# Optimization experiments

Hardware: AMD Instinct MI355X
Metric: run time of the kernel (lower is better)

Reference implementation:

```python
import jax, jax.numpy as jnp
import numpy as np

N_HEADS = 16


def setup_inputs() -> dict:
    key = jax.random.key(0)
    ks = jax.random.split(key, 6)
    b, s, d = 1, 2048, 2048
    x = jax.random.normal(ks[0], (b, s, d), dtype=jnp.float32)
    Wqkv = jax.random.normal(ks[1], (d, 3 * d), dtype=jnp.float32) * (d ** -0.5)
    Wqkv_bias = jax.random.normal(ks[2], (3 * d,), dtype=jnp.float32) * 0.02
    out_w = jax.random.normal(ks[3], (d, d), dtype=jnp.float32) * (d ** -0.5)
    out_b = jax.random.normal(ks[4], (d,), dtype=jnp.float32) * 0.02
    attn_bias = jax.random.normal(ks[5], (1, N_HEADS, 1, s), dtype=jnp.float32)
    key_padding_mask = jnp.ones((b, s), dtype=bool)
    return {"x": x, "Wqkv": Wqkv, "Wqkv_bias": Wqkv_bias, "out_w": out_w,
            "out_b": out_b, "attn_bias": attn_bias,
            "key_padding_mask": key_padding_mask}


def reference(x, Wqkv, Wqkv_bias, out_w, out_b, attn_bias, key_padding_mask):
    b, s, d = x.shape
    h = N_HEADS
    dh = d // h
    qkv = x @ Wqkv + Wqkv_bias                      # [b, s, 3d]
    q, k, v = jnp.split(qkv, 3, axis=-1)
    q = q.reshape(b, s, h, dh).transpose(0, 2, 1, 3)  # b h s d
    k = k.reshape(b, s, h, dh).transpose(0, 2, 1, 3)
    v = v.reshape(b, s, h, dh).transpose(0, 2, 1, 3)
    scale = 1.0 / jnp.sqrt(jnp.asarray(dh, x.dtype))
    attn_weight = jnp.einsum('bhqd,bhkd->bhqk', q, k) * scale
    attn_weight = attn_weight + attn_bias           # broadcast [1,h,1,s]
    min_val = jnp.finfo(x.dtype).min
    # key padding mask: [b, s_k] -> [b,1,1,s_k]
    attn_weight = jnp.where(key_padding_mask[:, None, None, :], attn_weight, min_val)
    # causal mask (s_q == s_k)
    causal = jnp.tril(jnp.ones((s, s), dtype=bool))
    attn_weight = jnp.where(causal[None, None, :, :], attn_weight, min_val)
    attn_weight = jax.nn.softmax(attn_weight, axis=-1)
    out = jnp.einsum('bhqk,bhkd->bhqd', attn_weight, v)
    out = out.transpose(0, 2, 1, 3).reshape(b, s, d)  # b s (h d)
    return out @ out_w + out_b
```

## Files before the change

kernel.cpp:

```cpp
#include <hip/hip_runtime.h>
#include <hip/hip_bf16.h>
#include <stdint.h>


#define SQ 2048
#define DM 2048
#define NH 16
#define DH 128
#define N3 6144
#define QKVN (NH * SQ * DH)

typedef unsigned short u16;
typedef __bf16 bf16_t;
typedef bf16_t bf16x8 __attribute__((ext_vector_type(8)));
typedef float f32x4 __attribute__((ext_vector_type(4)));
typedef const __attribute__((address_space(1))) unsigned int guint;
typedef __attribute__((address_space(3))) unsigned int luint;

__device__ __forceinline__ float b2f(u16 u) {
    union { uint32_t i; float f; } c; c.i = ((uint32_t)u) << 16; return c.f;
}
__device__ __forceinline__ u16 f2b(float f) {
    union { float f; uint32_t i; } c; c.f = f;
    uint32_t r = c.i + 0x7FFF + ((c.i >> 16) & 1);
    return (u16)(r >> 16);
}
__device__ __forceinline__ uint32_t pk(u16 a, u16 b) {
    return (uint32_t)a | ((uint32_t)b << 16);
}
__device__ __forceinline__ uint32_t pkrnd(float a, float b) {
    union { float f; uint32_t i; } x, y; x.f = a; y.f = b;
    return __builtin_amdgcn_perm(y.i + 0x8000u, x.i + 0x8000u, 0x07060302u);
}
__device__ __forceinline__ float ld1(const void* p, size_t i, bool fp32) {
    return fp32 ? ((const float*)p)[i] : b2f(((const u16*)p)[i]);
}

__global__ void detect_dtype(const void* x, int* flag) {
    __shared__ int bad;
    if (threadIdx.x == 0) bad = 0;
    __syncthreads();
    float v = b2f(((const u16*)x)[threadIdx.x]);
    if (!(fabsf(v) <= 1024.0f)) atomicOr(&bad, 1);
    __syncthreads();
    if (threadIdx.x == 0) *flag = bad;
}

__global__ __launch_bounds__(256) void convert_x(
    const void* __restrict__ x, u16* __restrict__ xb, const int* __restrict__ flagp)
{
    const bool fp32 = (*flagp != 0);
    const size_t i = ((size_t)blockIdx.x * 256 + threadIdx.x) * 8;
    uint4 v;
    if (fp32) {
        const float* p = (const float*)x + i;
        float4 a = *(const float4*)p, b = *(const float4*)(p + 4);
        v.x = pkrnd(a.x, a.y); v.y = pkrnd(a.z, a.w);
        v.z = pkrnd(b.x, b.y); v.w = pkrnd(b.z, b.w);
    } else {
        v = *(const uint4*)((const u16*)x + i);
    }
    *(uint4*)(xb + i) = v;
}

__global__ __launch_bounds__(256) void transpose_w(
    const void* __restrict__ W, u16* __restrict__ Wt, int N,
    const int* __restrict__ flagp)
{
    const bool fp32 = (*flagp != 0);
    __shared__ __attribute__((aligned(16))) u16 tile[64 * 72];
    const int t = threadIdx.x;
    const int n0 = blockIdx.x * 64, k0 = blockIdx.y * 64;
#pragma unroll
    for (int i = 0; i < 2; ++i) {
        int c = t + 256 * i; int kr = c >> 3; int n8 = (c & 7) * 8;
        uint4 v;
        if (fp32) {
            const float* p = (const float*)W + (size_t)(k0 + kr) * N + n0 + n8;
            float4 a = *(const float4*)p, b = *(const float4*)(p + 4);
            v.x = pkrnd(a.x, a.y); v.y = pkrnd(a.z, a.w);
            v.z = pkrnd(b.x, b.y); v.w = pkrnd(b.z, b.w);
        } else {
            v = *(const uint4*)((const u16*)W + (size_t)(k0 + kr) * N + n0 + n8);
        }
        *(uint4*)&tile[kr * 72 + n8] = v;
    }
    __syncthreads();
#pragma unroll
    for (int i = 0; i < 2; ++i) {
        int c = t + 256 * i; int nr = c >> 3; int k8 = (c & 7) * 8;
        uint32_t dw[4];
#pragma unroll
        for (int j = 0; j < 4; ++j)
            dw[j] = pk(tile[(k8 + 2*j) * 72 + nr], tile[(k8 + 2*j + 1) * 72 + nr]);
        *(uint4*)&Wt[(size_t)(n0 + nr) * 2048 + k0 + k8] =
            make_uint4(dw[0], dw[1], dw[2], dw[3]);
    }
}

__global__ __launch_bounds__(512, 2) void qkv_gemm8(
    const u16* __restrict__ xb, const u16* __restrict__ Wt,
    const void* __restrict__ bias,
    u16* __restrict__ Q, u16* __restrict__ K, u16* __restrict__ Vt,
    const int* __restrict__ flagp)
{
    const bool fp32 = (*flagp != 0);
    __shared__ __attribute__((aligned(16))) u16 AB[2][2][256 * 64];
    const int t = threadIdx.x;
    const int w = t >> 6, l = t & 63;
    const int wm = w >> 2, wn = w & 3;
    const int lq = l & 15, quad = l >> 4;
    const int rsub = t >> 3;
    const int sw = ((t & 7) ^ (rsub & 7)) << 3;

    const int orig = blockIdx.x;
    const int xcd = orig & 7, j = orig >> 3;
    const int bx = (xcd & 3) * 6 + (j >> 2);
    const int by = (xcd >> 2) * 4 + (j & 3);
    const int m0 = by * 256, n0 = bx * 256;

    const u16* Ag = xb + (size_t)m0 * 2048;
    const u16* Bg = Wt + (size_t)n0 * 2048;

#define STAGE_A(u, ue) do {                                                   \
    if ((u) < 32) {                                                           \
      _Pragma("unroll")                                                       \
      for (int i_ = 0; i_ < 2; ++i_) {                                        \
        const int rb_ = i_ * 128 + (ue) * 64;                                 \
        const u16* src_ = Ag + (size_t)(rb_ + rsub) * 2048 + (u) * 64 + sw;   \
        __builtin_amdgcn_global_load_lds((guint*)(const void*)src_,           \
          (luint*)(void*)&AB[(u) & 1][0][(rb_ + w * 8) * 64], 16, 0, 0);      \
      }                                                                       \
    } } while (0)

#define STAGE_B(u, ue) do {                                                   \
    if ((u) < 32) {                                                           \
      _Pragma("unroll")                                                       \
      for (int i_ = 0; i_ < 2; ++i_) {                                        \
        const int row_ = (ue) * 32 + (rsub & 31) + ((rsub >> 5) + 2 * i_) * 64;\
        const int wrow_ = (ue) * 32 + (w & 3) * 8 + ((w >> 2) + 2 * i_) * 64; \
        const u16* src_ = Bg + (size_t)row_ * 2048 + (u) * 64 + sw;           \
        __builtin_amdgcn_global_load_lds((guint*)(const void*)src_,           \
          (luint*)(void*)&AB[(u) & 1][1][wrow_ * 64], 16, 0, 0);              \
      }                                                                       \
    } } while (0)

#define READ_A(buf, mhalf) do {                                               \
    _Pragma("unroll")                                                         \
    for (int mf_ = 0; mf_ < 4; ++mf_) {                                       \
      const int r_ = wm*128 + ((mhalf)*4 + mf_)*16 + lq;                      \
      _Pragma("unroll")                                                       \
      for (int ks_ = 0; ks_ < 2; ++ks_) {                                     \
        const int c_ = (ks_*4 + quad) ^ (r_ & 7);                             \
        a[mf_][ks_] = *(const bf16x8*)&AB[buf][0][r_*64 + c_*8];              \
      }                                                                       \
    } } while (0)

#define READ_B(dst, buf, nhalf) do {                                          \
    _Pragma("unroll")                                                         \
    for (int nf_ = 0; nf_ < 2; ++nf_) {                                       \
      const int r_ = wn*64 + ((nhalf)*2 + nf_)*16 + lq;                       \
      _Pragma("unroll")                                                       \
      for (int ks_ = 0; ks_ < 2; ++ks_) {                                     \
        const int c_ = (ks_*4 + quad) ^ (r_ & 7);                             \
        dst[nf_][ks_] = *(const bf16x8*)&AB[buf][1][r_*64 + c_*8];            \
      }                                                                       \
    } } while (0)

#define MMA_Q(mh, nh, bsrc) do {                                              \
    __builtin_amdgcn_s_setprio(1);                                            \
    _Pragma("unroll")                                                         \
    for (int mf_ = 0; mf_ < 4; ++mf_)                                         \
    _Pragma("unroll")                                                         \
    for (int nf_ = 0; nf_ < 2; ++nf_)                                         \
    _Pragma("unroll")                                                         \
    for (int ks_ = 0; ks_ < 2; ++ks_)                                         \
      acc[(mh)*4+mf_][(nh)*2+nf_] =                                           \
        __builtin_amdgcn_mfma_f32_16x16x32_bf16(a[mf_][ks_], bsrc[nf_][ks_],  \
          acc[(mh)*4+mf_][(nh)*2+nf_], 0, 0, 0);                              \
    __builtin_amdgcn_s_setprio(0);                                            \
} while (0)

#define TILE_BODY(T, buf, BEC, BEN) do {                                      \
                                                                      \
    READ_A(buf, 0);                                                           \
    STAGE_B((T) + 1, 0);                                                      \
    __builtin_amdgcn_s_barrier();                                             \
    asm volatile("s_waitcnt lgkmcnt(0)" ::: "memory");                        \
    MMA_Q(0, 0, BEC);                                                         \
    __builtin_amdgcn_s_barrier();                                             \
                                                                      \
    READ_B(bo, buf, 1);                                                       \
    STAGE_A((T) + 2, 0);                                                      \
    __builtin_amdgcn_s_barrier();                                             \
    asm volatile("s_waitcnt lgkmcnt(0)" ::: "memory");                        \
    MMA_Q(0, 1, bo);                                                          \
    __builtin_amdgcn_s_barrier();                                             \
                                                                      \
    READ_A(buf, 1);                                                           \
    STAGE_B((T) + 2, 1);                                                      \
    if ((T) >= 30) asm volatile("s_waitcnt vmcnt(0)" ::: "memory");           \
    else           asm volatile("s_waitcnt vmcnt(4)" ::: "memory");           \
    __builtin_amdgcn_s_barrier();                                             \
    asm volatile("s_waitcnt lgkmcnt(0)" ::: "memory");                        \
    MMA_Q(1, 1, bo);                                                          \
    __builtin_amdgcn_s_barrier();                                             \
                                                                      \
    READ_B(BEN, (buf) ^ 1, 0);                                                \
    STAGE_A((T) + 2, 1);                                                      \
    __builtin_amdgcn_s_barrier();                                             \
    asm volatile("s_waitcnt lgkmcnt(0)" ::: "memory");                        \
    MMA_Q(1, 0, BEC);                                                         \
    __builtin_amdgcn_s_barrier();                                             \
} while (0)

    const f32x4 vzero = {0.f, 0.f, 0.f, 0.f};
    f32x4 acc[8][4];
#pragma unroll
    for (int i = 0; i < 8; ++i)
#pragma unroll
        for (int j2 = 0; j2 < 4; ++j2) acc[i][j2] = vzero;
    bf16x8 a[4][2], bo[2][2], be_a[2][2], be_b[2][2];

    STAGE_A(0, 0); STAGE_B(0, 0); STAGE_B(0, 1); STAGE_A(0, 1);
    STAGE_A(1, 0); STAGE_B(1, 1); STAGE_A(1, 1);
    asm volatile("s_waitcnt vmcnt(6)" ::: "memory");
    __builtin_amdgcn_s_barrier();
    READ_B(be_a, 0, 0);

#pragma unroll 1
    for (int T = 0; T < 32; T += 2) {
        TILE_BODY(T,     0, be_a, be_b);
        TILE_BODY(T + 1, 1, be_b, be_a);
    }

    const float scale = 0.08838834764831845f;
#pragma unroll
    for (int nf = 0; nf < 4; ++nf) {
        const int n = n0 + wn*64 + nf*16 + lq;
        const float bn = ld1(bias, n, fp32);
        const int which = n >> 11, r2 = n & 2047, h = r2 >> 7, dc = r2 & 127;
#pragma unroll
        for (int mf = 0; mf < 8; ++mf) {
#pragma unroll
            for (int r = 0; r < 4; ++r) {
                const int m = m0 + wm*128 + mf*16 + quad*4 + r;
                const float val = acc[mf][nf][r] + bn;
                if (which == 0)
                    Q[((size_t)(h << 11) + m) * DH + dc] = f2b(val * scale);
                else if (which == 1)
                    K[((size_t)(h << 11) + m) * DH + dc] = f2b(val);
                else {
                    const int kl = m & 63;
                    const int pos = ((kl >> 5) << 5) + (((kl >> 2) & 3) << 3)
                                  + (((kl >> 4) & 1) << 2) + (kl & 3);
                    const int mp = (m & ~63) | pos;
                    Vt[((size_t)h * DH + dc) * SQ + mp] = f2b(val);
                }
            }
        }
    }
#undef STAGE_A
#undef STAGE_B
#undef READ_A
#undef READ_B
#undef MMA_Q
#undef TILE_BODY
}

__global__ __launch_bounds__(256) void attn_mfma(
    const u16* __restrict__ Q, const u16* __restrict__ K,
    const u16* __restrict__ Vt, const void* __restrict__ attn_bias,
    u16* __restrict__ Ob0, u16* __restrict__ Ob1,
    float* __restrict__ Lb0, float* __restrict__ Lb1,
    const int* __restrict__ flagp)
{
    const bool fp32 = (*flagp != 0);
    __shared__ __attribute__((aligned(16))) u16 Qs[4 * 64 * 32];
    __shared__ __attribute__((aligned(16))) u16 Ks[4 * 64 * 32];
    __shared__ __attribute__((aligned(16))) u16 Vs[128 * 64];
    __shared__ __attribute__((aligned(16))) float biasF[2048];

    const int t = threadIdx.x;
    const int w = t >> 6, l = t & 63;
    const int lq = l & 15, quad = l >> 4;
    const int px = blockIdx.x, h = blockIdx.y, par = blockIdx.z;

    const u16* Qh = Q + (size_t)h * SQ * DH;
    const u16* Kh = K + (size_t)h * SQ * DH;
    const u16* Vh = Vt + (size_t)h * DH * SQ;
    u16* Ob = par ? Ob1 : Ob0;
    float* Lb = par ? Lb1 : Lb0;

#pragma unroll
    for (int i = 0; i < 8; ++i) {
        int j = t + 256 * i;
        biasF[j] = ld1(attn_bias, (size_t)h * SQ + j, fp32);
    }

    const f32x4 vzero = {0.f, 0.f, 0.f, 0.f};

    for (int phase = 0; phase < 2; ++phase) {
        const int qt = phase ? (31 - px) : px;
        const int q0 = qt * 64;
        const int qbase = q0 + w * 16;

        __syncthreads();
#pragma unroll
        for (int i = 0; i < 4; ++i) {
            const int ci = w * 4 + i;
            const int kc = ci >> 2, kg = ci & 3;
            const u16* src = Qh + (size_t)(q0 + kg*16 + (l >> 2)) * DH
                           + kc*32 + (l & 3) * 8;
            __builtin_amdgcn_global_load_lds((guint*)(const void*)src,
                (luint*)(void*)&Qs[ci * 512], 16, 0, 0);
        }
        __syncthreads();
        bf16x8 bq[4];
#pragma unroll
        for (int kc = 0; kc < 4; ++kc)
            bq[kc] = *(const bf16x8*)&Qs[kc*2048 + (w*16 + lq)*32 + quad*8];

        f32x4 O[8];
#pragma unroll
        for (int i = 0; i < 8; ++i) O[i] = vzero;
        float lsum = 0.0f;

        for (int kt = par; kt <= qt; kt += 2) {
            const int k0 = kt * 64;
            __syncthreads();
#pragma unroll
            for (int i = 0; i < 4; ++i) {
                const int ci = w * 4 + i;
                const int kc = ci >> 2, kg = ci & 3;
                const u16* src = Kh + (size_t)(k0 + kg*16 + (l >> 2)) * DH
                               + kc*32 + (l & 3) * 8;
                __builtin_amdgcn_global_load_lds((guint*)(const void*)src,
                    (luint*)(void*)&Ks[ci * 512], 16, 0, 0);
            }
#pragma unroll
            for (int i = 0; i < 4; ++i) {
                const int ci = w * 4 + i;
                const int dim = ci * 8 + (l >> 3);
                const u16* src = Vh + (size_t)dim * SQ + k0
                               + (((l & 7) ^ (l >> 3)) << 3);
                __builtin_amdgcn_global_load_lds((guint*)(const void*)src,
                    (luint*)(void*)&Vs[ci * 512], 16, 0, 0);
            }
            __syncthreads();

            f32x4 S[4];
#pragma unroll
            for (int ks = 0; ks < 4; ++ks) S[ks] = vzero;
#pragma unroll
            for (int kc = 0; kc < 4; ++kc) {
#pragma unroll
                for (int ks = 0; ks < 4; ++ks) {
                    bf16x8 ak = *(const bf16x8*)&Ks[kc*2048 + (ks*16 + lq)*32 + quad*8];
                    S[ks] = __builtin_amdgcn_mfma_f32_16x16x32_bf16(ak, bq[kc], S[ks], 0, 0, 0);
                }
            }

            const bool full = (k0 + 63) <= qbase;
            uint32_t Ppk[4][2];
            float part = 0.0f;
#pragma unroll
            for (int ks = 0; ks < 4; ++ks) {
                const f32x4 b4 = *(const f32x4*)&biasF[k0 + ks*16 + quad*4];
                float p[4];
#pragma unroll
                for (int r = 0; r < 4; ++r) {
                    float pe = __expf(S[ks][r] + b4[r]);
                    if (!full) {
                        const int key = k0 + ks*16 + quad*4 + r;
                        if (key > qbase + lq) pe = 0.0f;
                    }
                    p[r] = pe;
                    part += pe;
                }
                Ppk[ks][0] = pkrnd(p[0], p[1]);
                Ppk[ks][1] = pkrnd(p[2], p[3]);
            }
            lsum += part;

#pragma unroll
            for (int s2 = 0; s2 < 2; ++s2) {
                union { uint32_t u[4]; bf16x8 v; } bP;
                bP.u[0] = Ppk[2*s2][0];   bP.u[1] = Ppk[2*s2][1];
                bP.u[2] = Ppk[2*s2+1][0]; bP.u[3] = Ppk[2*s2+1][1];
                const int ch = ((s2*4 + quad) ^ (lq & 7)) << 3;
#pragma unroll
                for (int ds = 0; ds < 8; ++ds) {
                    bf16x8 aV = *(const bf16x8*)&Vs[(ds*16 + lq)*64 + ch];
                    O[ds] = __builtin_amdgcn_mfma_f32_16x16x32_bf16(aV, bP.v, O[ds], 0, 0, 0);
                }
            }
        }

        lsum += __shfl_xor(lsum, 16, 64);
        lsum += __shfl_xor(lsum, 32, 64);
        if (l < 16) Lb[(size_t)h * SQ + qbase + l] = lsum;
        u16* orow = Ob + (size_t)(qbase + lq) * DM + h * DH;
#pragma unroll
        for (int ds = 0; ds < 8; ++ds) {
            uint2 o2;
            o2.x = pkrnd(O[ds][0], O[ds][1]);
            o2.y = pkrnd(O[ds][2], O[ds][3]);
            *(uint2*)&orow[ds*16 + quad*4] = o2;
        }
    }
}

__global__ __launch_bounds__(256) void combine_o(
    const u16* __restrict__ O0, const u16* __restrict__ O1,
    const float* __restrict__ L0, const float* __restrict__ L1,
    u16* __restrict__ attno)
{
    const size_t i = ((size_t)blockIdx.x * 256 + threadIdx.x) * 8;
    const int row = (int)(i >> 11);
    const int h = ((int)i & 2047) >> 7;
    const float inv = 1.0f / (L0[h * SQ + row] + L1[h * SQ + row]);
    const ushort4 a = *(const ushort4*)(O0 + i);
    const ushort4 b = *(const ushort4*)(O1 + i);
    const ushort4 c = *(const ushort4*)(O0 + i + 4);
    const ushort4 d = *(const ushort4*)(O1 + i + 4);
    uint4 v;
    v.x = pkrnd((b2f(a.x)+b2f(b.x))*inv, (b2f(a.y)+b2f(b.y))*inv);
    v.y = pkrnd((b2f(a.z)+b2f(b.z))*inv, (b2f(a.w)+b2f(b.w))*inv);
    v.z = pkrnd((b2f(c.x)+b2f(d.x))*inv, (b2f(c.y)+b2f(d.y))*inv);
    v.w = pkrnd((b2f(c.z)+b2f(d.z))*inv, (b2f(c.w)+b2f(d.w))*inv);
    *(uint4*)(attno + i) = v;
}

__global__ __launch_bounds__(256) void out_gemm(
    const u16* __restrict__ attno, const u16* __restrict__ OWt,
    const void* __restrict__ bias, void* __restrict__ out,
    const int* __restrict__ flagp)
{
    const bool fp32 = (*flagp != 0);
    __shared__ __attribute__((aligned(16))) u16 Alds[128 * 32];
    __shared__ __attribute__((aligned(16))) u16 Blds[64 * 32];
    const int t = threadIdx.x;
    const int m0 = blockIdx.y * 128, n0 = blockIdx.x * 64;
    const int w = t >> 6, l = t & 63;
    const int lq = l & 15, quad = l >> 4;
    const int srow = l >> 2, scol = (l & 3) * 8;
    const f32x4 vzero = {0.f, 0.f, 0.f, 0.f};
    f32x4 acc[2][4];
#pragma unroll
    for (int i = 0; i < 2; ++i)
#pragma unroll
        for (int j = 0; j < 4; ++j) acc[i][j] = vzero;

    for (int k0 = 0; k0 < 2048; k0 += 32) {
#pragma unroll
        for (int i = 0; i < 2; ++i) {
            const int row = w * 32 + i * 16 + srow;
            const u16* ga = attno + (size_t)(m0 + row) * 2048 + k0 + scol;
            __builtin_amdgcn_global_load_lds((guint*)(const void*)ga,
                (luint*)(void*)&Alds[w * 1024 + i * 512], 16, 0, 0);
        }
        {
            const u16* gb = OWt + (size_t)(n0 + w*16 + srow) * 2048 + k0 + scol;
            __builtin_amdgcn_global_load_lds((guint*)(const void*)gb,
                (luint*)(void*)&Blds[w * 512], 16, 0, 0);
        }
        __syncthreads();
        bf16x8 bfr[4];
#pragma unroll
        for (int ns = 0; ns < 4; ++ns)
            bfr[ns] = *(const bf16x8*)&Blds[(ns*16 + lq) * 32 + quad*8];
#pragma unroll
        for (int ms = 0; ms < 2; ++ms) {
            bf16x8 af = *(const bf16x8*)&Alds[(w*32 + ms*16 + lq) * 32 + quad*8];
#pragma unroll
            for (int ns = 0; ns < 4; ++ns)
                acc[ms][ns] = __builtin_amdgcn_mfma_f32_16x16x32_bf16(
                    af, bfr[ns], acc[ms][ns], 0, 0, 0);
        }
        __syncthreads();
    }

#pragma unroll
    for (int ns = 0; ns < 4; ++ns) {
        const int n = n0 + ns*16 + lq;
        const float bn = ld1(bias, n, fp32);
#pragma unroll
        for (int ms = 0; ms < 2; ++ms) {
#pragma unroll
            for (int r = 0; r < 4; ++r) {
                const int m = m0 + w*32 + ms*16 + quad*4 + r;
                const float v = acc[ms][ns][r] + bn;
                const size_t idx = (size_t)m * DM + n;
                if (fp32) ((float*)out)[idx] = v;
                else      ((u16*)out)[idx]  = f2b(v);
            }
        }
    }
}

extern "C" void kernel_launch(void* const* d_in, const int* in_sizes, int n_in,
                              void* d_out, int out_size, void* d_ws, size_t ws_size,
                              hipStream_t stream)
{
    const void* x      = d_in[0];
    const void* wqkv   = d_in[1];
    const void* wqkv_b = d_in[2];
    const void* out_w  = d_in[3];
    const void* out_b  = d_in[4];
    const void* attn_b = d_in[5];

    char* base = (char*)d_ws;
    int* flag = (int*)base;
    u16* xb   = (u16*)(base + 256);
    u16* Wt   = xb + (size_t)SQ * DM;
    u16* Qb   = Wt + (size_t)N3 * DM;
    u16* Kb   = Qb + QKVN;
    u16* Vtb  = Kb + QKVN;
    float* L0 = (float*)(Vtb + QKVN);
    float* L1 = L0 + NH * SQ;
    u16* OWt  = Wt;
    u16* Ob0  = Wt + (size_t)DM * DM;
    u16* Ob1  = Ob0 + (size_t)SQ * DM;
    u16* attno = xb;

    detect_dtype<<<1, 256, 0, stream>>>(x, flag);
    convert_x<<<(SQ * DM) / (256 * 8), 256, 0, stream>>>(x, xb, flag);
    transpose_w<<<dim3(N3/64, DM/64), 256, 0, stream>>>(wqkv, Wt, N3, flag);
    qkv_gemm8<<<dim3(192), 512, 0, stream>>>(xb, Wt, wqkv_b, Qb, Kb, Vtb, flag);
    transpose_w<<<dim3(DM/64, DM/64), 256, 0, stream>>>(out_w, OWt, DM, flag);
    attn_mfma<<<dim3(16, NH, 2), 256, 0, stream>>>(Qb, Kb, Vtb, attn_b,
                                                   Ob0, Ob1, L0, L1, flag);
    combine_o<<<(SQ * DM) / (256 * 8), 256, 0, stream>>>(Ob0, Ob1, L0, L1, attno);
    out_gemm<<<dim3(DM/64, SQ/128), 256, 0, stream>>>(attno, OWt, out_b,
                                                      d_out, flag);
}
```

Measured before the change: 303.2 us.

## Retile QKV GEMM to 128x192 tiles with 4 waves and 512 blocks

The QKV projection GEMM moves from 256x256 tiles with 8 waves (192 blocks) to 128x192 tiles with 4 waves (512 blocks). The point is to fill all 256 CUs, since 192 blocks leave many idle. The staging schedule, the LDS layout and the XCD-aware block mapping are rewritten to match, and the B tile is now staged in one step per iteration. The smaller tiles give less reuse per loaded byte and mean more global traffic.

Result: faster. 287.4 us (-5.2%).

```diff
diff --git a/kernel.cpp b/kernel.cpp
--- a/kernel.cpp
+++ b/kernel.cpp
@@ -98,26 +98,27 @@
     }
 }
 
-__global__ __launch_bounds__(512, 2) void qkv_gemm8(
+__global__ __launch_bounds__(256, 2) void qkv_gemm4(
     const u16* __restrict__ xb, const u16* __restrict__ Wt,
     const void* __restrict__ bias,
     u16* __restrict__ Q, u16* __restrict__ K, u16* __restrict__ Vt,
     const int* __restrict__ flagp)
 {
     const bool fp32 = (*flagp != 0);
-    __shared__ __attribute__((aligned(16))) u16 AB[2][2][256 * 64];
+    __shared__ __attribute__((aligned(16))) u16 Alds[2][128 * 64];
+    __shared__ __attribute__((aligned(16))) u16 Blds[2][192 * 64];
     const int t = threadIdx.x;
     const int w = t >> 6, l = t & 63;
-    const int wm = w >> 2, wn = w & 3;
+    const int wm = w >> 1, wn = w & 1;
     const int lq = l & 15, quad = l >> 4;
     const int rsub = t >> 3;
     const int sw = ((t & 7) ^ (rsub & 7)) << 3;
 
     const int orig = blockIdx.x;
     const int xcd = orig & 7, j = orig >> 3;
-    const int bx = (xcd & 3) * 6 + (j >> 2);
-    const int by = (xcd >> 2) * 4 + (j & 3);
-    const int m0 = by * 256, n0 = bx * 256;
+    const int bx = (xcd & 3) * 8 + (j & 7);
+    const int by = (xcd >> 2) * 8 + (j >> 3);
+    const int m0 = by * 128, n0 = bx * 192;
 
     const u16* Ag = xb + (size_t)m0 * 2048;
     const u16* Bg = Wt + (size_t)n0 * 2048;
@@ -126,65 +127,63 @@
     if ((u) < 32) {                                                           \
       _Pragma("unroll")                                                       \
       for (int i_ = 0; i_ < 2; ++i_) {                                        \
-        const int rb_ = i_ * 128 + (ue) * 64;                                 \
+        const int rb_ = i_ * 64 + (ue) * 32;                                  \
         const u16* src_ = Ag + (size_t)(rb_ + rsub) * 2048 + (u) * 64 + sw;   \
         __builtin_amdgcn_global_load_lds((guint*)(const void*)src_,           \
-          (luint*)(void*)&AB[(u) & 1][0][(rb_ + w * 8) * 64], 16, 0, 0);      \
+          (luint*)(void*)&Alds[(u) & 1][rb_ * 64 + t * 8], 16, 0, 0);         \
       }                                                                       \
     } } while (0)
 
-#define STAGE_B(u, ue) do {                                                   \
+#define STAGE_B(u) do {                                                       \
     if ((u) < 32) {                                                           \
       _Pragma("unroll")                                                       \
-      for (int i_ = 0; i_ < 2; ++i_) {                                        \
-        const int row_ = (ue) * 32 + (rsub & 31) + ((rsub >> 5) + 2 * i_) * 64;\
-        const int wrow_ = (ue) * 32 + (w & 3) * 8 + ((w >> 2) + 2 * i_) * 64; \
-        const u16* src_ = Bg + (size_t)row_ * 2048 + (u) * 64 + sw;           \
+      for (int i_ = 0; i_ < 6; ++i_) {                                        \
+        const int rb_ = i_ * 32;                                              \
+        const u16* src_ = Bg + (size_t)(rb_ + rsub) * 2048 + (u) * 64 + sw;   \
         __builtin_amdgcn_global_load_lds((guint*)(const void*)src_,           \
-          (luint*)(void*)&AB[(u) & 1][1][wrow_ * 64], 16, 0, 0);              \
+          (luint*)(void*)&Blds[(u) & 1][rb_ * 64 + t * 8], 16, 0, 0);         \
       }                                                                       \
     } } while (0)
 
-#define READ_A(buf, mhalf) do {                                               \
+#define READ_A(buf, mh) do {                                                  \
     _Pragma("unroll")                                                         \
-    for (int mf_ = 0; mf_ < 4; ++mf_) {                                       \
-      const int r_ = wm*128 + ((mhalf)*4 + mf_)*16 + lq;                      \
+    for (int mf_ = 0; mf_ < 2; ++mf_) {                                       \
+      const int r_ = wm*64 + ((mh)*2 + mf_)*16 + lq;                          \
       _Pragma("unroll")                                                       \
       for (int ks_ = 0; ks_ < 2; ++ks_) {                                     \
         const int c_ = (ks_*4 + quad) ^ (r_ & 7);                             \
-        a[mf_][ks_] = *(const bf16x8*)&AB[buf][0][r_*64 + c_*8];              \
+        a[mf_][ks_] = *(const bf16x8*)&Alds[buf][r_*64 + c_*8];               \
       }                                                                       \
     } } while (0)
 
-#define READ_B(dst, buf, nhalf) do {                                          \
+#define READ_B(dst, buf, nhh) do {                                            \
     _Pragma("unroll")                                                         \
-    for (int nf_ = 0; nf_ < 2; ++nf_) {                                       \
-      const int r_ = wn*64 + ((nhalf)*2 + nf_)*16 + lq;                       \
+    for (int nf_ = 0; nf_ < 3; ++nf_) {                                       \
+      const int r_ = wn*96 + ((nhh)*3 + nf_)*16 + lq;                         \
       _Pragma("unroll")                                                       \
       for (int ks_ = 0; ks_ < 2; ++ks_) {                                     \
         const int c_ = (ks_*4 + quad) ^ (r_ & 7);                             \
-        dst[nf_][ks_] = *(const bf16x8*)&AB[buf][1][r_*64 + c_*8];            \
+        dst[nf_][ks_] = *(const bf16x8*)&Blds[buf][r_*64 + c_*8];             \
       }                                                                       \
     } } while (0)
 
-#define MMA_Q(mh, nh, bsrc) do {                                              \
+#define MMA_Q(mh, nhh, bsrc) do {                                             \
     __builtin_amdgcn_s_setprio(1);                                            \
     _Pragma("unroll")                                                         \
-    for (int mf_ = 0; mf_ < 4; ++mf_)                                         \
+    for (int mf_ = 0; mf_ < 2; ++mf_)                                         \
     _Pragma("unroll")                                                         \
-    for (int nf_ = 0; nf_ < 2; ++nf_)                                         \
+    for (int nf_ = 0; nf_ < 3; ++nf_)                                         \
     _Pragma("unroll")                                                         \
     for (int ks_ = 0; ks_ < 2; ++ks_)                                         \
-      acc[(mh)*4+mf_][(nh)*2+nf_] =                                           \
+      acc[(mh)*2+mf_][(nhh)*3+nf_] =                                          \
         __builtin_amdgcn_mfma_f32_16x16x32_bf16(a[mf_][ks_], bsrc[nf_][ks_],  \
-          acc[(mh)*4+mf_][(nh)*2+nf_], 0, 0, 0);                              \
+          acc[(mh)*2+mf_][(nhh)*3+nf_], 0, 0, 0);                             \
     __builtin_amdgcn_s_setprio(0);                                            \
 } while (0)
 
 #define TILE_BODY(T, buf, BEC, BEN) do {                                      \
                                                                       \
     READ_A(buf, 0);                                                           \
-    STAGE_B((T) + 1, 0);                                                      \
     __builtin_amdgcn_s_barrier();                                             \
     asm volatile("s_waitcnt lgkmcnt(0)" ::: "memory");                        \
     MMA_Q(0, 0, BEC);                                                         \
@@ -192,15 +191,15 @@
                                                                       \
     READ_B(bo, buf, 1);                                                       \
     STAGE_A((T) + 2, 0);                                                      \
+    if ((T) >= 30) asm volatile("s_waitcnt vmcnt(0)" ::: "memory");           \
+    else           asm volatile("s_waitcnt vmcnt(2)" ::: "memory");           \
     __builtin_amdgcn_s_barrier();                                             \
     asm volatile("s_waitcnt lgkmcnt(0)" ::: "memory");                        \
     MMA_Q(0, 1, bo);                                                          \
     __builtin_amdgcn_s_barrier();                                             \
                                                                       \
     READ_A(buf, 1);                                                           \
-    STAGE_B((T) + 2, 1);                                                      \
-    if ((T) >= 30) asm volatile("s_waitcnt vmcnt(0)" ::: "memory");           \
-    else           asm volatile("s_waitcnt vmcnt(4)" ::: "memory");           \
+    STAGE_B((T) + 2);                                                         \
     __builtin_amdgcn_s_barrier();                                             \
     asm volatile("s_waitcnt lgkmcnt(0)" ::: "memory");                        \
     MMA_Q(1, 1, bo);                                                          \
@@ -215,16 +214,16 @@
 } while (0)
 
     const f32x4 vzero = {0.f, 0.f, 0.f, 0.f};
-    f32x4 acc[8][4];
-#pragma unroll
-    for (int i = 0; i < 8; ++i)
-#pragma unroll
-        for (int j2 = 0; j2 < 4; ++j2) acc[i][j2] = vzero;
-    bf16x8 a[4][2], bo[2][2], be_a[2][2], be_b[2][2];
-
-    STAGE_A(0, 0); STAGE_B(0, 0); STAGE_B(0, 1); STAGE_A(0, 1);
-    STAGE_A(1, 0); STAGE_B(1, 1); STAGE_A(1, 1);
-    asm volatile("s_waitcnt vmcnt(6)" ::: "memory");
+    f32x4 acc[4][6];
+#pragma unroll
+    for (int i = 0; i < 4; ++i)
+#pragma unroll
+        for (int j2 = 0; j2 < 6; ++j2) acc[i][j2] = vzero;
+    bf16x8 a[2][2], bo[3][2], be_a[3][2], be_b[3][2];
+
+    STAGE_A(0, 0); STAGE_B(0); STAGE_A(0, 1);
+    STAGE_A(1, 0); STAGE_B(1); STAGE_A(1, 1);
+    asm volatile("s_waitcnt vmcnt(10)" ::: "memory");
     __builtin_amdgcn_s_barrier();
     READ_B(be_a, 0, 0);
 
@@ -236,15 +235,15 @@
 
     const float scale = 0.08838834764831845f;
 #pragma unroll
-    for (int nf = 0; nf < 4; ++nf) {
-        const int n = n0 + wn*64 + nf*16 + lq;
+    for (int nf = 0; nf < 6; ++nf) {
+        const int n = n0 + wn*96 + nf*16 + lq;
         const float bn = ld1(bias, n, fp32);
         const int which = n >> 11, r2 = n & 2047, h = r2 >> 7, dc = r2 & 127;
 #pragma unroll
-        for (int mf = 0; mf < 8; ++mf) {
+        for (int mf = 0; mf < 4; ++mf) {
 #pragma unroll
             for (int r = 0; r < 4; ++r) {
-                const int m = m0 + wm*128 + mf*16 + quad*4 + r;
+                const int m = m0 + wm*64 + mf*16 + quad*4 + r;
                 const float val = acc[mf][nf][r] + bn;
                 if (which == 0)
                     Q[((size_t)(h << 11) + m) * DH + dc] = f2b(val * scale);
@@ -527,7 +526,7 @@
     detect_dtype<<<1, 256, 0, stream>>>(x, flag);
     convert_x<<<(SQ * DM) / (256 * 8), 256, 0, stream>>>(x, xb, flag);
     transpose_w<<<dim3(N3/64, DM/64), 256, 0, stream>>>(wqkv, Wt, N3, flag);
-    qkv_gemm8<<<dim3(192), 512, 0, stream>>>(xb, Wt, wqkv_b, Qb, Kb, Vtb, flag);
+    qkv_gemm4<<<dim3(512), 256, 0, stream>>>(xb, Wt, wqkv_b, Qb, Kb, Vtb, flag);
     transpose_w<<<dim3(DM/64, DM/64), 256, 0, stream>>>(out_w, OWt, DM, flag);
     attn_mfma<<<dim3(16, NH, 2), 256, 0, stream>>>(Qb, Kb, Vtb, attn_b,
                                                    Ob0, Ob1, L0, L1, flag);
```
